# Kernel optimization log

Hardware: AMD Instinct MI355X
Metric: run time of the kernel (lower is better)

## Reference

```python
import jax, jax.numpy as jnp
import numpy as np

B, T, IN, OUT = 4, 8192, 512, 512
DIM, G, V, D = 32, 8, 8, 64  # quantizer dim, groups, num_vars, var_dim (vq_dim//groups)
TAU = 2.0  # initial gumbel temperature temp[0]
EPS = 1e-10


def setup_inputs() -> dict:
    key = jax.random.key(0)
    ks = jax.random.split(key, 8)
    s = lambda k, sh, f: (jax.random.normal(k, sh, jnp.float32) * f)
    return {
        "x": s(ks[0], (B, T, IN), 1.0),
        "W_pre": s(ks[1], (IN, DIM), IN ** -0.5),
        "b_pre": jnp.zeros((DIM,), jnp.float32),
        "W_proj": s(ks[2], (DIM, G * V), DIM ** -0.5),
        "b_proj": jnp.zeros((G * V,), jnp.float32),
        "codebook": s(ks[3], (G, V, D), 1.0),
        "W_post": s(ks[4], (G * D, OUT), (G * D) ** -0.5),
        "b_post": jnp.zeros((OUT,), jnp.float32),
        "u": jax.random.uniform(ks[5], (B, T, G, V), jnp.float32),
    }


def reference(x, W_pre, b_pre, W_proj, b_proj, codebook, W_post, b_post, u):
    b, t, _ = x.shape
    g, v, d = codebook.shape
    # pre-projection to quantizer dim, then logits over groups x num_vars
    h = x @ W_pre + b_pre                                # (B,T,32)
    logits = (h @ W_proj + b_proj).reshape(b, t, g, v)   # (B,T,G,V)
    # gumbel-softmax (hard, straight-through) as in F.gumbel_softmax
    gum = -jnp.log(-jnp.log(u + EPS) + EPS)
    y_soft = jax.nn.softmax((logits + gum) / TAU, axis=-1)
    hard = jax.nn.one_hot(jnp.argmax(y_soft, axis=-1), v, dtype=y_soft.dtype)
    w = hard + y_soft - jax.lax.stop_gradient(y_soft)    # (B,T,G,V)
    # codebook lookup: weighted sum over num_vars per group, concat groups
    q = jnp.einsum("btgv,gvd->btgd", w, codebook).reshape(b, t, g * d)
    return q @ W_post + b_post                           # (B,T,OUT)
```

## Files before the change

### kernel.cpp

```cpp
#include <hip/hip_runtime.h>
#include <hip/hip_bf16.h>
#include <stdint.h>
#include <stddef.h>

#define BT_TOK   32768
#define IN_DIM   512
#define OUT_DIM  512
#define QDIM     32
#define NG       8
#define NV       8
#define VD       64
#define EPS_G    1e-10f

#define MT       64

__global__ __launch_bounds__(256) void build_p2(
    const float* __restrict__ codebook,
    const float* __restrict__ W_post,
    __hip_bfloat16* __restrict__ P2)
{
    const int b  = blockIdx.x;
    const int p  = b >> 6;
    const int ij = b & 63;
    const int i  = ij >> 3, j = ij & 7;
    const int t  = threadIdx.x;

    const float* ca  = codebook + ((size_t)(2 * p) * NV + i) * VD;
    const float* cbp = codebook + ((size_t)(2 * p + 1) * NV + j) * VD;
    const float* wa  = W_post + (size_t)(2 * p) * VD * OUT_DIM;
    const float* wb  = W_post + (size_t)(2 * p + 1) * VD * OUT_DIM;

    float a0 = 0.f, a1 = 0.f;
#pragma unroll 8
    for (int d = 0; d < VD; ++d) {
        const float sa = ca[d];
        const float sb = cbp[d];
        a0 += sa * wa[(size_t)d * OUT_DIM + t]       + sb * wb[(size_t)d * OUT_DIM + t];
        a1 += sa * wa[(size_t)d * OUT_DIM + t + 256] + sb * wb[(size_t)d * OUT_DIM + t + 256];
    }
    __hip_bfloat16* dst = P2 + ((size_t)(p * 64 + ij)) * OUT_DIM;
    dst[t]       = __float2bfloat16(a0);
    dst[t + 256] = __float2bfloat16(a1);
}

__global__ __launch_bounds__(256, 3) void fused_main(
    const float* __restrict__ x,
    const float* __restrict__ W_pre,
    const float* __restrict__ b_pre,
    const float* __restrict__ W_proj,
    const float* __restrict__ b_proj,
    const float* __restrict__ u,
    const float* __restrict__ b_post,
    const __hip_bfloat16* __restrict__ P2,
    float* __restrict__ out)
{
    __shared__ float Hs4[4][MT][36];
    __shared__ int   pidx_s[4][MT];

    const int t    = threadIdx.x;
    const int lane = t & 63;
    const int w    = __builtin_amdgcn_readfirstlane(t >> 6);
    const int tokbase = blockIdx.x * MT;
    const int gtok    = tokbase + lane;

    float acc[QDIM];
#pragma unroll
    for (int j = 0; j < QDIM; ++j) acc[j] = 0.f;

    const float* xrow = x + (size_t)gtok * IN_DIM + w * 128;

    for (int c = 0; c < 4; ++c) {
        float4 xr[8];
#pragma unroll
        for (int f = 0; f < 8; ++f)
            xr[f] = ((const float4*)xrow)[c * 8 + f];

        const float* wbase = W_pre + (size_t)(w * 128 + c * 32) * QDIM;
#pragma unroll
        for (int kk = 0; kk < 32; ++kk) {
            const float xv = ((const float*)xr)[kk];
            const float4* wr = (const float4*)(wbase + (size_t)kk * QDIM);
            const float4 w0 = wr[0], w1 = wr[1], w2 = wr[2], w3 = wr[3];
            const float4 w4 = wr[4], w5 = wr[5], w6 = wr[6], w7 = wr[7];
            acc[0]  += xv * w0.x; acc[1]  += xv * w0.y; acc[2]  += xv * w0.z; acc[3]  += xv * w0.w;
            acc[4]  += xv * w1.x; acc[5]  += xv * w1.y; acc[6]  += xv * w1.z; acc[7]  += xv * w1.w;
            acc[8]  += xv * w2.x; acc[9]  += xv * w2.y; acc[10] += xv * w2.z; acc[11] += xv * w2.w;
            acc[12] += xv * w3.x; acc[13] += xv * w3.y; acc[14] += xv * w3.z; acc[15] += xv * w3.w;
            acc[16] += xv * w4.x; acc[17] += xv * w4.y; acc[18] += xv * w4.z; acc[19] += xv * w4.w;
            acc[20] += xv * w5.x; acc[21] += xv * w5.y; acc[22] += xv * w5.z; acc[23] += xv * w5.w;
            acc[24] += xv * w6.x; acc[25] += xv * w6.y; acc[26] += xv * w6.z; acc[27] += xv * w6.w;
            acc[28] += xv * w7.x; acc[29] += xv * w7.y; acc[30] += xv * w7.z; acc[31] += xv * w7.w;
        }
    }

#pragma unroll
    for (int j4 = 0; j4 < 8; ++j4)
        *(float4*)&Hs4[w][lane][j4 * 4] =
            make_float4(acc[j4 * 4], acc[j4 * 4 + 1], acc[j4 * 4 + 2], acc[j4 * 4 + 3]);
    __syncthreads();

#pragma unroll
    for (int r = 0; r < 8; ++r) {
        const int id  = t + 256 * r;
        const int tok = id >> 5;
        const int j   = id & 31;
        const float h = b_pre[j] + Hs4[0][tok][j] + Hs4[1][tok][j]
                                 + Hs4[2][tok][j] + Hs4[3][tok][j];
        Hs4[0][tok][j] = h;
    }
    __syncthreads();

    float h[QDIM];
#pragma unroll
    for (int j4 = 0; j4 < 8; ++j4) {
        const float4 v = *(const float4*)&Hs4[0][lane][j4 * 4];
        h[j4 * 4] = v.x; h[j4 * 4 + 1] = v.y; h[j4 * 4 + 2] = v.z; h[j4 * 4 + 3] = v.w;
    }

    int idx2[2];
#pragma unroll
    for (int gg = 0; gg < 2; ++gg) {
        const int g = 2 * w + gg;
        const float4 b0 = *(const float4*)&b_proj[g * 8];
        const float4 b1 = *(const float4*)&b_proj[g * 8 + 4];
        float lg[8] = {b0.x, b0.y, b0.z, b0.w, b1.x, b1.y, b1.z, b1.w};

#pragma unroll
        for (int j = 0; j < QDIM; ++j) {
            const float hv = h[j];
            const float4 a0 = *(const float4*)&W_proj[(size_t)j * 64 + g * 8];
            const float4 a1 = *(const float4*)&W_proj[(size_t)j * 64 + g * 8 + 4];
            lg[0] += hv * a0.x; lg[1] += hv * a0.y; lg[2] += hv * a0.z; lg[3] += hv * a0.w;
            lg[4] += hv * a1.x; lg[5] += hv * a1.y; lg[6] += hv * a1.z; lg[7] += hv * a1.w;
        }

        const float4 u0 = *(const float4*)&u[(size_t)gtok * 64 + g * 8];
        const float4 u1 = *(const float4*)&u[(size_t)gtok * 64 + g * 8 + 4];
        float y[8];
        y[0] = lg[0] - logf(-logf(u0.x + EPS_G) + EPS_G);
        y[1] = lg[1] - logf(-logf(u0.y + EPS_G) + EPS_G);
        y[2] = lg[2] - logf(-logf(u0.z + EPS_G) + EPS_G);
        y[3] = lg[3] - logf(-logf(u0.w + EPS_G) + EPS_G);
        y[4] = lg[4] - logf(-logf(u1.x + EPS_G) + EPS_G);
        y[5] = lg[5] - logf(-logf(u1.y + EPS_G) + EPS_G);
        y[6] = lg[6] - logf(-logf(u1.z + EPS_G) + EPS_G);
        y[7] = lg[7] - logf(-logf(u1.w + EPS_G) + EPS_G);

        float best = y[0];
        int bi = 0;
#pragma unroll
        for (int v = 1; v < 8; ++v)
            if (y[v] > best) { best = y[v]; bi = v; }
        idx2[gg] = bi;
    }
    pidx_s[w][lane] = idx2[0] * 8 + idx2[1];
    __syncthreads();

    const int o2 = t * 2;
    const float bp0 = b_post[o2];
    const float bp1 = b_post[o2 + 1];
    float* orow = out + (size_t)tokbase * OUT_DIM;
    const uint32_t* p2u = (const uint32_t*)P2;

#pragma unroll 4
    for (int tok = 0; tok < MT; ++tok) {
        const int p0 = pidx_s[0][tok];
        const int p1 = pidx_s[1][tok];
        const int p2i = pidx_s[2][tok];
        const int p3 = pidx_s[3][tok];
        const uint32_t r0 = p2u[(size_t)(0 * 64 + p0) * 256 + t];
        const uint32_t r1 = p2u[(size_t)(1 * 64 + p1) * 256 + t];
        const uint32_t r2 = p2u[(size_t)(2 * 64 + p2i) * 256 + t];
        const uint32_t r3 = p2u[(size_t)(3 * 64 + p3) * 256 + t];
        float s0 = bp0, s1 = bp1;
        s0 += __uint_as_float(r0 << 16); s1 += __uint_as_float(r0 & 0xffff0000u);
        s0 += __uint_as_float(r1 << 16); s1 += __uint_as_float(r1 & 0xffff0000u);
        s0 += __uint_as_float(r2 << 16); s1 += __uint_as_float(r2 & 0xffff0000u);
        s0 += __uint_as_float(r3 << 16); s1 += __uint_as_float(r3 & 0xffff0000u);
        *(float2*)&orow[(size_t)tok * OUT_DIM + o2] = make_float2(s0, s1);
    }
}

extern "C" void kernel_launch(void* const* d_in, const int* in_sizes, int n_in,
                              void* d_out, int out_size, void* d_ws, size_t ws_size,
                              hipStream_t stream) {
    const float* x        = (const float*)d_in[0];
    const float* W_pre    = (const float*)d_in[1];
    const float* b_pre    = (const float*)d_in[2];
    const float* W_proj   = (const float*)d_in[3];
    const float* b_proj   = (const float*)d_in[4];
    const float* codebook = (const float*)d_in[5];
    const float* W_post   = (const float*)d_in[6];
    const float* b_post   = (const float*)d_in[7];
    const float* u        = (const float*)d_in[8];
    float* out = (float*)d_out;

    __hip_bfloat16* P2 = (__hip_bfloat16*)d_ws;

    build_p2<<<256, 256, 0, stream>>>(codebook, W_post, P2);
    fused_main<<<BT_TOK / MT, 256, 0, stream>>>(x, W_pre, b_pre, W_proj, b_proj,
                                                u, b_post, P2, out);
}
```

Baseline: 169.6 us.

## Use 8 waves per block, splitting the K reduction and output tokens

The main kernel now runs 512 threads per block with 8 wavefronts. Each wave reduces a 64-wide slice of the input dimension instead of 128, computes one quantizer group instead of two, and the block's output writes are split across two token halves. The aim is more waves in flight per block and a shorter serial chain per thread, which helps hide memory latency on the x stream. In exchange the block needs more shared memory for partial sums, adds a reduction pass and an extra barrier, and launch bounds of 512 threads with 4 blocks may tighten register limits.

```diff
diff --git a/kernel.cpp b/kernel.cpp
--- a/kernel.cpp
+++ b/kernel.cpp
@@ -13,6 +13,7 @@
 #define EPS_G    1e-10f
 
 #define MT       64
+#define NW       8
 
 __global__ __launch_bounds__(256) void build_p2(
     const float* __restrict__ codebook,
@@ -43,7 +44,7 @@
     dst[t + 256] = __float2bfloat16(a1);
 }
 
-__global__ __launch_bounds__(256, 3) void fused_main(
+__global__ __launch_bounds__(512, 4) void fused_main(
     const float* __restrict__ x,
     const float* __restrict__ W_pre,
     const float* __restrict__ b_pre,
@@ -54,7 +55,8 @@
     const __hip_bfloat16* __restrict__ P2,
     float* __restrict__ out)
 {
-    __shared__ float Hs4[4][MT][36];
+    __shared__ float Hs4[NW][MT][36];
+    __shared__ int   idxs_s[NG][MT];
     __shared__ int   pidx_s[4][MT];
 
     const int t    = threadIdx.x;
@@ -67,15 +69,16 @@
 #pragma unroll
     for (int j = 0; j < QDIM; ++j) acc[j] = 0.f;
 
-    const float* xrow = x + (size_t)gtok * IN_DIM + w * 128;
-
-    for (int c = 0; c < 4; ++c) {
+    const float* xrow = x + (size_t)gtok * IN_DIM + w * 64;
+
+#pragma unroll
+    for (int c = 0; c < 2; ++c) {
         float4 xr[8];
 #pragma unroll
         for (int f = 0; f < 8; ++f)
             xr[f] = ((const float4*)xrow)[c * 8 + f];
 
-        const float* wbase = W_pre + (size_t)(w * 128 + c * 32) * QDIM;
+        const float* wbase = W_pre + (size_t)(w * 64 + c * 32) * QDIM;
 #pragma unroll
         for (int kk = 0; kk < 32; ++kk) {
             const float xv = ((const float*)xr)[kk];
@@ -100,12 +103,13 @@
     __syncthreads();
 
 #pragma unroll
-    for (int r = 0; r < 8; ++r) {
-        const int id  = t + 256 * r;
+    for (int r = 0; r < 4; ++r) {
+        const int id  = t + 512 * r;
         const int tok = id >> 5;
         const int j   = id & 31;
-        const float h = b_pre[j] + Hs4[0][tok][j] + Hs4[1][tok][j]
-                                 + Hs4[2][tok][j] + Hs4[3][tok][j];
+        float h = b_pre[j];
+#pragma unroll
+        for (int q = 0; q < NW; ++q) h += Hs4[q][tok][j];
         Hs4[0][tok][j] = h;
     }
     __syncthreads();
@@ -117,10 +121,8 @@
         h[j4 * 4] = v.x; h[j4 * 4 + 1] = v.y; h[j4 * 4 + 2] = v.z; h[j4 * 4 + 3] = v.w;
     }
 
-    int idx2[2];
-#pragma unroll
-    for (int gg = 0; gg < 2; ++gg) {
-        const int g = 2 * w + gg;
+    {
+        const int g = w;
         const float4 b0 = *(const float4*)&b_proj[g * 8];
         const float4 b1 = *(const float4*)&b_proj[g * 8 + 4];
         float lg[8] = {b0.x, b0.y, b0.z, b0.w, b1.x, b1.y, b1.z, b1.w};
@@ -151,33 +153,41 @@
 #pragma unroll
         for (int v = 1; v < 8; ++v)
             if (y[v] > best) { best = y[v]; bi = v; }
-        idx2[gg] = bi;
-    }
-    pidx_s[w][lane] = idx2[0] * 8 + idx2[1];
-    __syncthreads();
-
-    const int o2 = t * 2;
+        idxs_s[g][lane] = bi;
+    }
+    __syncthreads();
+
+    if (t < 256) {
+        const int p = t >> 6, tok = t & 63;
+        pidx_s[p][tok] = idxs_s[2 * p][tok] * 8 + idxs_s[2 * p + 1][tok];
+    }
+    __syncthreads();
+
+    const int tokhalf = t >> 8;
+    const int tt = t & 255;
+    const int o2 = tt * 2;
     const float bp0 = b_post[o2];
     const float bp1 = b_post[o2 + 1];
-    float* orow = out + (size_t)tokbase * OUT_DIM;
+    float* orow = out + (size_t)(tokbase + tokhalf * 32) * OUT_DIM;
     const uint32_t* p2u = (const uint32_t*)P2;
 
 #pragma unroll 4
-    for (int tok = 0; tok < MT; ++tok) {
+    for (int tok0 = 0; tok0 < 32; ++tok0) {
+        const int tok = tokhalf * 32 + tok0;
         const int p0 = pidx_s[0][tok];
         const int p1 = pidx_s[1][tok];
         const int p2i = pidx_s[2][tok];
         const int p3 = pidx_s[3][tok];
-        const uint32_t r0 = p2u[(size_t)(0 * 64 + p0) * 256 + t];
-        const uint32_t r1 = p2u[(size_t)(1 * 64 + p1) * 256 + t];
-        const uint32_t r2 = p2u[(size_t)(2 * 64 + p2i) * 256 + t];
-        const uint32_t r3 = p2u[(size_t)(3 * 64 + p3) * 256 + t];
+        const uint32_t r0 = p2u[(size_t)(0 * 64 + p0) * 256 + tt];
+        const uint32_t r1 = p2u[(size_t)(1 * 64 + p1) * 256 + tt];
+        const uint32_t r2 = p2u[(size_t)(2 * 64 + p2i) * 256 + tt];
+        const uint32_t r3 = p2u[(size_t)(3 * 64 + p3) * 256 + tt];
         float s0 = bp0, s1 = bp1;
         s0 += __uint_as_float(r0 << 16); s1 += __uint_as_float(r0 & 0xffff0000u);
         s0 += __uint_as_float(r1 << 16); s1 += __uint_as_float(r1 & 0xffff0000u);
         s0 += __uint_as_float(r2 << 16); s1 += __uint_as_float(r2 & 0xffff0000u);
         s0 += __uint_as_float(r3 << 16); s1 += __uint_as_float(r3 & 0xffff0000u);
-        *(float2*)&orow[(size_t)tok * OUT_DIM + o2] = make_float2(s0, s1);
+        *(float2*)&orow[(size_t)tok0 * OUT_DIM + o2] = make_float2(s0, s1);
     }
 }
 
@@ -198,6 +208,6 @@
     __hip_bfloat16* P2 = (__hip_bfloat16*)d_ws;
 
     build_p2<<<256, 256, 0, stream>>>(codebook, W_post, P2);
-    fused_main<<<BT_TOK / MT, 256, 0, stream>>>(x, W_pre, b_pre, W_proj, b_proj,
+    fused_main<<<BT_TOK / MT, 512, 0, stream>>>(x, W_pre, b_pre, W_proj, b_proj,
                                                 u, b_post, P2, out);
 }
```

After: 159.9 us. 1.06x faster.

## Coalesce x loads via LDS staging with register prefetch; widen output stores to float4

Applied to the files above, without the earlier changes.

Each wave now loads x in a coalesced pattern, with 8 lanes covering one token's 32-float chunk, and transposes it through shared memory. Before, each lane strided through its own token row. The next chunk is prefetched into registers while the current one is computed, to overlap global latency with the FMA loop. The output phase now writes float4 stores of 4 outputs, with two tokens handled per iteration across block halves, and the launch-bound occupancy hint is raised from 3 to 4. The costs are added LDS traffic, an extra barrier and more register pressure under the tighter launch bound.

```diff
diff --git a/kernel.cpp b/kernel.cpp
--- a/kernel.cpp
+++ b/kernel.cpp
@@ -13,6 +13,7 @@
 #define EPS_G    1e-10f
 
 #define MT       64
+#define NW       4
 
 __global__ __launch_bounds__(256) void build_p2(
     const float* __restrict__ codebook,
@@ -43,7 +44,7 @@
     dst[t + 256] = __float2bfloat16(a1);
 }
 
-__global__ __launch_bounds__(256, 3) void fused_main(
+__global__ __launch_bounds__(256, 4) void fused_main(
     const float* __restrict__ x,
     const float* __restrict__ W_pre,
     const float* __restrict__ b_pre,
@@ -54,7 +55,8 @@
     const __hip_bfloat16* __restrict__ P2,
     float* __restrict__ out)
 {
-    __shared__ float Hs4[4][MT][36];
+    __shared__ float Xs[NW][MT][36];
+    __shared__ int   idxs_s[NG][MT];
     __shared__ int   pidx_s[4][MT];
 
     const int t    = threadIdx.x;
@@ -67,13 +69,31 @@
 #pragma unroll
     for (int j = 0; j < QDIM; ++j) acc[j] = 0.f;
 
-    const float* xrow = x + (size_t)gtok * IN_DIM + w * 128;
+    const int stok = lane >> 3;
+    const int sf   = lane & 7;
+    const float* xsl = x + (size_t)tokbase * IN_DIM + w * 128;
+
+    float4 xg[8];
+#pragma unroll
+    for (int i = 0; i < 8; ++i)
+        xg[i] = *(const float4*)(xsl + (size_t)(i * 8 + stok) * IN_DIM + sf * 4);
 
     for (int c = 0; c < 4; ++c) {
+#pragma unroll
+        for (int i = 0; i < 8; ++i)
+            *(float4*)&Xs[w][i * 8 + stok][sf * 4] = xg[i];
+
+        if (c < 3) {
+#pragma unroll
+            for (int i = 0; i < 8; ++i)
+                xg[i] = *(const float4*)(xsl + (size_t)(i * 8 + stok) * IN_DIM
+                                              + (c + 1) * 32 + sf * 4);
+        }
+
         float4 xr[8];
 #pragma unroll
         for (int f = 0; f < 8; ++f)
-            xr[f] = ((const float4*)xrow)[c * 8 + f];
+            xr[f] = *(const float4*)&Xs[w][lane][f * 4];
 
         const float* wbase = W_pre + (size_t)(w * 128 + c * 32) * QDIM;
 #pragma unroll
@@ -93,9 +113,10 @@
         }
     }
 
+    __syncthreads();
 #pragma unroll
     for (int j4 = 0; j4 < 8; ++j4)
-        *(float4*)&Hs4[w][lane][j4 * 4] =
+        *(float4*)&Xs[w][lane][j4 * 4] =
             make_float4(acc[j4 * 4], acc[j4 * 4 + 1], acc[j4 * 4 + 2], acc[j4 * 4 + 3]);
     __syncthreads();
 
@@ -104,20 +125,19 @@
         const int id  = t + 256 * r;
         const int tok = id >> 5;
         const int j   = id & 31;
-        const float h = b_pre[j] + Hs4[0][tok][j] + Hs4[1][tok][j]
-                                 + Hs4[2][tok][j] + Hs4[3][tok][j];
-        Hs4[0][tok][j] = h;
+        const float h = b_pre[j] + Xs[0][tok][j] + Xs[1][tok][j]
+                                 + Xs[2][tok][j] + Xs[3][tok][j];
+        Xs[0][tok][j] = h;
     }
     __syncthreads();
 
     float h[QDIM];
 #pragma unroll
     for (int j4 = 0; j4 < 8; ++j4) {
-        const float4 v = *(const float4*)&Hs4[0][lane][j4 * 4];
+        const float4 v = *(const float4*)&Xs[0][lane][j4 * 4];
         h[j4 * 4] = v.x; h[j4 * 4 + 1] = v.y; h[j4 * 4 + 2] = v.z; h[j4 * 4 + 3] = v.w;
     }
 
-    int idx2[2];
 #pragma unroll
     for (int gg = 0; gg < 2; ++gg) {
         const int g = 2 * w + gg;
@@ -151,33 +171,43 @@
 #pragma unroll
         for (int v = 1; v < 8; ++v)
             if (y[v] > best) { best = y[v]; bi = v; }
-        idx2[gg] = bi;
-    }
-    pidx_s[w][lane] = idx2[0] * 8 + idx2[1];
-    __syncthreads();
-
-    const int o2 = t * 2;
-    const float bp0 = b_post[o2];
-    const float bp1 = b_post[o2 + 1];
-    float* orow = out + (size_t)tokbase * OUT_DIM;
-    const uint32_t* p2u = (const uint32_t*)P2;
+        idxs_s[g][lane] = bi;
+    }
+    __syncthreads();
+
+    {
+        const int p = t >> 6, tok = t & 63;
+        pidx_s[p][tok] = idxs_s[2 * p][tok] * 8 + idxs_s[2 * p + 1][tok];
+    }
+    __syncthreads();
+
+    const int half = t >> 7;
+    const int tt   = t & 127;
+    const int o4   = tt * 4;
+    const float4 bp = *(const float4*)&b_post[o4];
+    const uint2* p2v = (const uint2*)P2;
 
 #pragma unroll 4
-    for (int tok = 0; tok < MT; ++tok) {
+    for (int it = 0; it < 32; ++it) {
+        const int tok = 2 * it + half;
         const int p0 = pidx_s[0][tok];
         const int p1 = pidx_s[1][tok];
         const int p2i = pidx_s[2][tok];
         const int p3 = pidx_s[3][tok];
-        const uint32_t r0 = p2u[(size_t)(0 * 64 + p0) * 256 + t];
-        const uint32_t r1 = p2u[(size_t)(1 * 64 + p1) * 256 + t];
-        const uint32_t r2 = p2u[(size_t)(2 * 64 + p2i) * 256 + t];
-        const uint32_t r3 = p2u[(size_t)(3 * 64 + p3) * 256 + t];
-        float s0 = bp0, s1 = bp1;
-        s0 += __uint_as_float(r0 << 16); s1 += __uint_as_float(r0 & 0xffff0000u);
-        s0 += __uint_as_float(r1 << 16); s1 += __uint_as_float(r1 & 0xffff0000u);
-        s0 += __uint_as_float(r2 << 16); s1 += __uint_as_float(r2 & 0xffff0000u);
-        s0 += __uint_as_float(r3 << 16); s1 += __uint_as_float(r3 & 0xffff0000u);
-        *(float2*)&orow[(size_t)tok * OUT_DIM + o2] = make_float2(s0, s1);
+        const uint2 r0 = p2v[(size_t)(0 * 64 + p0) * 128 + tt];
+        const uint2 r1 = p2v[(size_t)(1 * 64 + p1) * 128 + tt];
+        const uint2 r2 = p2v[(size_t)(2 * 64 + p2i) * 128 + tt];
+        const uint2 r3 = p2v[(size_t)(3 * 64 + p3) * 128 + tt];
+        float4 s = bp;
+        s.x += __uint_as_float(r0.x << 16); s.y += __uint_as_float(r0.x & 0xffff0000u);
+        s.z += __uint_as_float(r0.y << 16); s.w += __uint_as_float(r0.y & 0xffff0000u);
+        s.x += __uint_as_float(r1.x << 16); s.y += __uint_as_float(r1.x & 0xffff0000u);
+        s.z += __uint_as_float(r1.y << 16); s.w += __uint_as_float(r1.y & 0xffff0000u);
+        s.x += __uint_as_float(r2.x << 16); s.y += __uint_as_float(r2.x & 0xffff0000u);
+        s.z += __uint_as_float(r2.y << 16); s.w += __uint_as_float(r2.y & 0xffff0000u);
+        s.x += __uint_as_float(r3.x << 16); s.y += __uint_as_float(r3.x & 0xffff0000u);
+        s.z += __uint_as_float(r3.y << 16); s.w += __uint_as_float(r3.y & 0xffff0000u);
+        *(float4*)&out[(size_t)(tokbase + tok) * OUT_DIM + o4] = s;
     }
 }
 
```

New measurement: 208.7 us. 23.0% more time.
